# Kernel optimization log

Measured on AMD Instinct MI355X. Metric: run time of the kernel, lower is better.

## Reference

```python
import jax, jax.numpy as jnp
import numpy as np

B, T, D = 2, 2048, 2048
H = 8
DK = 256   # head_qk_dim
DV = 512   # head_v_dim
C = 64     # retention chunk size
EPS = 1e-5
ROPE_BASE = 10000.0


def _rotary(x):
    # x: [B, T, H, DK], non-interleaved (rotate-half) rotary over full head dim
    half = DK // 2
    inv_freq = 1.0 / (ROPE_BASE ** (jnp.arange(0, DK, 2, dtype=jnp.float32) / DK))
    freqs = jnp.arange(T, dtype=jnp.float32)[:, None] * inv_freq[None, :]  # [T, half]
    cos = jnp.cos(freqs)[None, :, None, :].astype(x.dtype)
    sin = jnp.sin(freqs)[None, :, None, :].astype(x.dtype)
    x1, x2 = x[..., :half], x[..., half:]
    return jnp.concatenate([x1 * cos - x2 * sin, x2 * cos + x1 * sin], axis=-1)


def setup_inputs() -> dict:
    key = jax.random.key(0)
    ks = jax.random.split(key, 6)
    s = 2.0 ** (-2.5) * (2.0 / 2048.0) ** 0.5  # xavier_uniform-ish scale, gain 2^-2.5
    return {
        "hidden_states": jax.random.normal(ks[0], (B, T, D), jnp.float32),
        "Wq": jax.random.normal(ks[1], (H * DK, D), jnp.float32) * s,
        "Wk": jax.random.normal(ks[2], (H * DK, D), jnp.float32) * s,
        "Wv": jax.random.normal(ks[3], (H * DV, D), jnp.float32) * s,
        "Wg": jax.random.normal(ks[4], (H * DV, D), jnp.float32) * s,
        "Wo": jax.random.normal(ks[5], (D, H * DV), jnp.float32) * s,
        "g_norm_weight": jnp.ones((DV,), jnp.float32),
    }


def reference(hidden_states, Wq, Wk, Wv, Wg, Wo, g_norm_weight):
    x = hidden_states  # [B, T, D]
    q = (x @ Wq.T).reshape(B, T, H, DK)
    k = (x @ Wk.T).reshape(B, T, H, DK)
    q = _rotary(q)
    k = _rotary(k)
    q = q.transpose(0, 2, 1, 3) * (DK ** -0.5)        # [B, H, T, DK]
    k = k.transpose(0, 2, 1, 3)                       # [B, H, T, DK]
    v = (x @ Wv.T).reshape(B, T, H, DV).transpose(0, 2, 1, 3)  # [B, H, T, DV]

    # RetNet multi-scale per-head decay
    logb = jnp.log(1.0 - 2.0 ** (-5.0 - jnp.arange(H, dtype=jnp.float32)))  # [H]
    i = jnp.arange(C, dtype=jnp.float32)
    # intra-chunk decay mask b^{i-j} for i>=j: [H, C, C]
    Dmask = jnp.where(i[:, None] >= i[None, :],
                      jnp.exp(logb[:, None, None] * (i[:, None] - i[None, :])), 0.0)
    q_dec = jnp.exp(logb[:, None] * (i + 1.0))        # [H, C]  decay applied to q vs carried state
    k_dec = jnp.exp(logb[:, None] * (C - 1.0 - i))    # [H, C]  decay applied to k for state update
    chunk_dec = jnp.exp(logb * C)                     # [H]

    N = T // C
    qc = q.reshape(B, H, N, C, DK).transpose(2, 0, 1, 3, 4)  # [N, B, H, C, DK]
    kc = k.reshape(B, H, N, C, DK).transpose(2, 0, 1, 3, 4)
    vc = v.reshape(B, H, N, C, DV).transpose(2, 0, 1, 3, 4)

    def body(S, inp):
        qi, ki, vi = inp  # [B,H,C,DK], [B,H,C,DK], [B,H,C,DV]
        inter = jnp.einsum('bhcd,bhdv->bhcv', qi * q_dec[None, :, :, None], S)
        scores = jnp.einsum('bhcd,bhmd->bhcm', qi, ki) * Dmask[None]
        o = inter + jnp.einsum('bhcm,bhmv->bhcv', scores, vi)
        S_new = S * chunk_dec[None, :, None, None] + \
                jnp.einsum('bhcd,bhcv->bhdv', ki * k_dec[None, :, :, None], vi)
        return S_new, o

    S0 = jnp.zeros((B, H, DK, DV), x.dtype)
    _, oc = jax.lax.scan(body, S0, (qc, kc, vc))  # oc: [N, B, H, C, DV]
    o = oc.transpose(1, 2, 0, 3, 4).reshape(B, H, T, DV).transpose(0, 2, 1, 3)  # [B, T, H, DV]

    g = (x @ Wg.T).reshape(B, T, H, DV)
    # fused RMSNorm + swish gate (per head_v_dim)
    o_n = o * jax.lax.rsqrt(jnp.mean(o * o, axis=-1, keepdims=True) + EPS) * g_norm_weight
    o = o_n * (g * jax.nn.sigmoid(g))
    return o.reshape(B, T, H * DV) @ Wo.T  # [B, T, D]
```

## Files before the change

### kernel.cpp

```cpp
#include <hip/hip_runtime.h>


typedef unsigned short u16;
typedef unsigned int u32;
typedef short bf16x8 __attribute__((ext_vector_type(8)));
typedef short s16x4 __attribute__((ext_vector_type(4)));
typedef float f32x4 __attribute__((ext_vector_type(4)));
typedef u32 u32x2 __attribute__((ext_vector_type(2)));
typedef u32 u32x4 __attribute__((ext_vector_type(4)));

typedef __attribute__((address_space(3))) u32 lds_u32;
typedef __attribute__((address_space(1))) const u32 gbl_u32;

__device__ __forceinline__ float bf2f(u16 u) {
    union { u32 i; float f; } x; x.i = ((u32)u) << 16; return x.f;
}
__device__ __forceinline__ u16 f2bf(float f) {
    union { float f; u32 i; } x; x.f = f;
    u32 u = x.i;
    u += 0x7fffu + ((u >> 16) & 1u);
    return (u16)(u >> 16);
}
__device__ __forceinline__ f32x4 mfma16(bf16x8 a, bf16x8 b, f32x4 c) {
    return __builtin_amdgcn_mfma_f32_16x16x32_bf16(a, b, c, 0, 0, 0);
}
__device__ __forceinline__ void gload16(const u16* g, u16* lds) {
    __builtin_amdgcn_global_load_lds((gbl_u32*)(unsigned long long)g,
                                     (lds_u32*)(u32)(unsigned long long)lds, 16, 0, 0);
}

__global__ __launch_bounds__(256)
void cvt_bf16(const float* __restrict__ src, u16* __restrict__ dst)
{
    size_t i = ((size_t)blockIdx.x * 256 + threadIdx.x) * 8;
    f32x4 a = *(const f32x4*)(src + i);
    f32x4 b = *(const f32x4*)(src + i + 4);
    bf16x8 r;
#pragma unroll
    for (int j = 0; j < 4; j++) { r[j] = (short)f2bf(a[j]); r[j + 4] = (short)f2bf(b[j]); }
    *(bf16x8*)(dst + i) = r;
}

template<bool CF32>
__global__ __launch_bounds__(256, 2)
void gemm_bt(const u16* __restrict__ A, const u16* __restrict__ Bm,
             void* __restrict__ Cv, int N, int K)
{
    __shared__ u16 Ab[128 * 64];
    __shared__ u16 Bb[128 * 64];
    const int tid = threadIdx.x;
    const int lane = tid & 63, wave = tid >> 6;
    const int quad = lane >> 4, l16 = lane & 15;
    const int tn = blockIdx.x, tm = blockIdx.y;
    const int wr = wave >> 1, wc = wave & 1;

    f32x4 acc[4][4];
#pragma unroll
    for (int i = 0; i < 4; i++)
#pragma unroll
        for (int j = 0; j < 4; j++) acc[i][j] = (f32x4){0.f, 0.f, 0.f, 0.f};

    const u16* Abase = A + (size_t)tm * 128 * K;
    const u16* Bbase = Bm + (size_t)tn * 128 * K;
    const int rsub = lane >> 3, csub = (lane & 7) * 8;

    for (int k0 = 0; k0 < K; k0 += 64) {
        __syncthreads();
#pragma unroll
        for (int i = 0; i < 4; i++) {
            int chunk = wave * 4 + i;
            int r = chunk * 8 + rsub;
            gload16(Abase + (size_t)r * K + k0 + csub, Ab + chunk * 512);
            gload16(Bbase + (size_t)r * K + k0 + csub, Bb + chunk * 512);
        }
        __syncthreads();
#pragma unroll
        for (int kc = 0; kc < 2; kc++) {
            bf16x8 af[4], bfr[4];
#pragma unroll
            for (int mt = 0; mt < 4; mt++)
                af[mt] = *(const bf16x8*)(Ab + (wr * 64 + mt * 16 + l16) * 64 + kc * 32 + quad * 8);
#pragma unroll
            for (int nt = 0; nt < 4; nt++)
                bfr[nt] = *(const bf16x8*)(Bb + (wc * 64 + nt * 16 + l16) * 64 + kc * 32 + quad * 8);
#pragma unroll
            for (int mt = 0; mt < 4; mt++)
#pragma unroll
                for (int nt = 0; nt < 4; nt++)
                    acc[mt][nt] = mfma16(af[mt], bfr[nt], acc[mt][nt]);
        }
    }
    const int row0 = tm * 128 + wr * 64 + quad * 4;
    const int col0 = tn * 128 + wc * 64 + l16;
#pragma unroll
    for (int mt = 0; mt < 4; mt++)
#pragma unroll
        for (int nt = 0; nt < 4; nt++)
#pragma unroll
            for (int r = 0; r < 4; r++) {
                size_t idx = (size_t)(row0 + mt * 16 + r) * N + col0 + nt * 16;
                if constexpr (CF32) ((float*)Cv)[idx] = acc[mt][nt][r];
                else                ((u16*)Cv)[idx]   = f2bf(acc[mt][nt][r]);
            }
}

__global__ __launch_bounds__(512, 2)
void gemm256(const u16* __restrict__ A, const u16* __restrict__ Bm,
             u16* __restrict__ C, int N, int K)
{
    __shared__ __align__(16) u16 As[2][2][256 * 32];
    __shared__ __align__(16) u16 Bs[2][2][256 * 32];
    const int tid = threadIdx.x;
    const int lane = tid & 63, wave = tid >> 6;
    const int quad = lane >> 4, l16 = lane & 15;
    const int wm = wave >> 2, wn = wave & 3;
    const int tn = blockIdx.x, tm = blockIdx.y;
    const int NTm1 = K / 64 - 1;
    const u16* Abase = A + (size_t)tm * 256 * K;
    const u16* Bbase = Bm + (size_t)tn * 256 * K;
    const int gr = tid >> 2;
    const int gc = (tid & 3) * 8;
    const int wv64 = wave * 64;

    f32x4 acc[8][4];
#pragma unroll
    for (int i = 0; i < 8; i++)
#pragma unroll
        for (int j = 0; j < 4; j++) acc[i][j] = (f32x4){0.f, 0.f, 0.f, 0.f};

    bf16x8 bq[8];
    bf16x8 af[4];

#define STAGE(arr, bf, kc, Gb, kt) do {                                         \
    int kt_ = (kt); kt_ = (kt_ > NTm1) ? NTm1 : kt_;                            \
    const u16* s_ = (Gb) + (size_t)gr * K + (size_t)kt_ * 64 + (kc) * 32 + gc;  \
    gload16(s_,                 &arr[bf][kc][wv64 * 8]);                        \
    gload16(s_ + (size_t)128 * K, &arr[bf][kc][(512 + wv64) * 8]);              \
} while (0)

#define LDA(bf, kc, mg) do {                                                    \
    _Pragma("unroll")                                                           \
    for (int j = 0; j < 4; j++)                                                 \
        af[j] = *(const bf16x8*)&As[bf][kc][(wm * 128 + (mg) * 64 + j * 16 + l16) * 32 + quad * 8]; \
} while (0)

#define LDB(bf) do {                                                            \
    _Pragma("unroll")                                                           \
    for (int kc_ = 0; kc_ < 2; kc_++)                                           \
        _Pragma("unroll")                                                       \
        for (int n_ = 0; n_ < 4; n_++)                                          \
            bq[kc_ * 4 + n_] = *(const bf16x8*)&Bs[bf][kc_][(wn * 64 + n_ * 16 + l16) * 32 + quad * 8]; \
} while (0)

#define MM16(kc, mg) do {                                                       \
    _Pragma("unroll")                                                           \
    for (int j = 0; j < 4; j++)                                                 \
        _Pragma("unroll")                                                       \
        for (int n_ = 0; n_ < 4; n_++)                                          \
            acc[(mg) * 4 + j][n_] = mfma16(af[j], bq[(kc) * 4 + n_], acc[(mg) * 4 + j][n_]); \
} while (0)

#define BAR   __builtin_amdgcn_s_barrier()
#define LGKM0 asm volatile("s_waitcnt lgkmcnt(0)" ::: "memory")
#define VM6   asm volatile("s_waitcnt vmcnt(6)" ::: "memory")
#define PRIO1 __builtin_amdgcn_s_setprio(1)
#define PRIO0 __builtin_amdgcn_s_setprio(0)

    STAGE(Bs, 0, 0, Bbase, 0);
    STAGE(Bs, 0, 1, Bbase, 0);
    STAGE(As, 0, 0, Abase, 0);
    STAGE(As, 0, 1, Abase, 0);
    asm volatile("s_waitcnt vmcnt(4)" ::: "memory");
    STAGE(Bs, 1, 0, Bbase, 1);
    STAGE(Bs, 1, 1, Bbase, 1);
    STAGE(As, 1, 0, Abase, 1);
    asm volatile("s_waitcnt vmcnt(6)" ::: "memory");
    BAR;

    const int NI = K / 128;
    for (int it = 0; it < NI; ++it) {
        const int t0 = 2 * it;
        LDB(0); LDA(0, 0, 0); STAGE(As, 1, 1, Abase, t0 + 1);
        BAR; LGKM0; PRIO1; MM16(0, 0); PRIO0; BAR;
        LDA(0, 0, 1); STAGE(Bs, 0, 0, Bbase, t0 + 2);
        BAR; LGKM0; PRIO1; MM16(0, 1); PRIO0; BAR;
        LDA(0, 1, 0); STAGE(Bs, 0, 1, Bbase, t0 + 2);
        BAR; LGKM0; PRIO1; MM16(1, 0); PRIO0; BAR;
        LDA(0, 1, 1); STAGE(As, 0, 0, Abase, t0 + 2);
        BAR; LGKM0; PRIO1; MM16(1, 1); PRIO0; VM6; BAR;
        LDB(1); LDA(1, 0, 0); STAGE(As, 0, 1, Abase, t0 + 2);
        BAR; LGKM0; PRIO1; MM16(0, 0); PRIO0; BAR;
        LDA(1, 0, 1); STAGE(Bs, 1, 0, Bbase, t0 + 3);
        BAR; LGKM0; PRIO1; MM16(0, 1); PRIO0; BAR;
        LDA(1, 1, 0); STAGE(Bs, 1, 1, Bbase, t0 + 3);
        BAR; LGKM0; PRIO1; MM16(1, 0); PRIO0; BAR;
        LDA(1, 1, 1); STAGE(As, 1, 0, Abase, t0 + 3);
        BAR; LGKM0; PRIO1; MM16(1, 1); PRIO0; VM6; BAR;
    }
    asm volatile("s_waitcnt vmcnt(0)" ::: "memory");

    const int row0 = tm * 256 + wm * 128 + quad * 4;
    const int col0 = tn * 256 + wn * 64 + l16;
#pragma unroll
    for (int mt = 0; mt < 8; mt++)
#pragma unroll
        for (int nt = 0; nt < 4; nt++)
#pragma unroll
            for (int r = 0; r < 4; r++)
                C[(size_t)(row0 + mt * 16 + r) * N + col0 + nt * 16] = f2bf(acc[mt][nt][r]);

#undef STAGE
#undef LDA
#undef LDB
#undef MM16
#undef BAR
#undef LGKM0
#undef VM6
#undef PRIO1
#undef PRIO0
}

__global__ __launch_bounds__(256, 2)
void rotary_scores(u16* __restrict__ q, const u16* __restrict__ k,
                   u16* __restrict__ kT, u16* __restrict__ P)
{
    __shared__ u16 qS[64 * 264];
    __shared__ u16 kS[64 * 264];
    const int tid = threadIdx.x;
    const int lane = tid & 63, wave = tid >> 6;
    const int quad = lane >> 4, l16 = lane & 15;
    const int bx = blockIdx.x;
    const int bh = bx & 15, n = bx >> 4;
    const int b = bh >> 3, h = bh & 7;
    const int t0 = n * 64;

    const int row = tid >> 2;
    const int j0 = (tid & 3) * 32;
    const size_t rowbase = (size_t)(b * 2048 + t0 + row) * 4096 + h * 256;
    const float tpos = (float)(t0 + row);
#pragma unroll
    for (int i = 0; i < 4; i++) {
        int j = j0 + i * 8;
        bf16x8 x1 = *(const bf16x8*)(q + rowbase + j);
        bf16x8 x2 = *(const bf16x8*)(q + rowbase + j + 128);
        bf16x8 y1 = *(const bf16x8*)(k + rowbase + j);
        bf16x8 y2 = *(const bf16x8*)(k + rowbase + j + 128);
        bf16x8 o1, o2, p1, p2;
#pragma unroll
        for (int e = 0; e < 8; e++) {
            float inv = expf((-9.210340371976184f / 128.f) * (float)(j + e));
            float ang = tpos * inv;
            float sv = sinf(ang), cv = cosf(ang);
            float a = bf2f((u16)x1[e]), bb = bf2f((u16)x2[e]);
            o1[e] = (short)f2bf((a * cv - bb * sv) * 0.0625f);
            o2[e] = (short)f2bf((bb * cv + a * sv) * 0.0625f);
            float e1 = bf2f((u16)y1[e]), e2 = bf2f((u16)y2[e]);
            p1[e] = (short)f2bf(e1 * cv - e2 * sv);
            p2[e] = (short)f2bf(e2 * cv + e1 * sv);
        }
        *(bf16x8*)(q + rowbase + j)       = o1;
        *(bf16x8*)(q + rowbase + j + 128) = o2;
        *(bf16x8*)(qS + row * 264 + j)       = o1;
        *(bf16x8*)(qS + row * 264 + j + 128) = o2;
        *(bf16x8*)(kS + row * 264 + j)       = p1;
        *(bf16x8*)(kS + row * 264 + j + 128) = p2;
    }
    __syncthreads();

    const float logb = logf(1.0f - exp2f(-5.0f - (float)h));
    f32x4 sc[4];
#pragma unroll
    for (int i = 0; i < 4; i++) sc[i] = (f32x4){0.f, 0.f, 0.f, 0.f};
#pragma unroll
    for (int kc = 0; kc < 8; kc++) {
        bf16x8 af = *(const bf16x8*)(qS + (wave * 16 + l16) * 264 + kc * 32 + quad * 8);
#pragma unroll
        for (int mt = 0; mt < 4; mt++) {
            bf16x8 bk = *(const bf16x8*)(kS + (mt * 16 + l16) * 264 + kc * 32 + quad * 8);
            sc[mt] = mfma16(af, bk, sc[mt]);
        }
    }
    u16* Pb = P + ((size_t)(bh * 32 + n)) * 64 * 64;
#pragma unroll
    for (int r = 0; r < 4; r++) {
        int cr = wave * 16 + quad * 4 + r;
        float rowe = __expf(logb * (float)(cr - 63));
#pragma unroll
        for (int mt = 0; mt < 4; mt++) {
            int m = mt * 16 + l16;
            float val = (cr >= m) ? sc[mt][r] * rowe : 0.0f;
            Pb[cr * 64 + m] = f2bf(val);
        }
    }

    const int d = tid;
    u16* dst = kT + ((size_t)(bh * 256 + d)) * 2048 + t0;
#pragma unroll
    for (int g8 = 0; g8 < 8; g8++) {
        bf16x8 w;
#pragma unroll
        for (int e = 0; e < 8; e++) w[e] = (short)kS[(g8 * 8 + e) * 264 + d];
        *(bf16x8*)(dst + g8 * 8) = w;
    }
}

__global__ __launch_bounds__(512, 2)
void retention(const u16* __restrict__ Q, const u16* __restrict__ KT,
               const u16* __restrict__ V, const u16* __restrict__ P,
               u16* __restrict__ O)
{
    __shared__ u16 St[2][32 * 264];
    __shared__ u16 vsT[2][32 * 72];

    const int tid = threadIdx.x;
    const int lane = tid & 63, wave = tid >> 6;
    const int quad = lane >> 4, l16 = lane & 15;
    const int bx = blockIdx.x;
    const int bh = bx & 15, vt = bx >> 4;
    const int b = bh >> 3, h = bh & 7;
    const int cgrp = wave >> 1, vhalf = wave & 1;

    const float logb = logf(1.0f - exp2f(-5.0f - (float)h));
    const float cdec = __expf(logb * 64.0f);

    int cr[4];
    float qdecr[4];
#pragma unroll
    for (int r = 0; r < 4; r++) {
        cr[r] = cgrp * 16 + quad * 4 + r;
        qdecr[r] = __expf(logb * (float)(cr[r] + 1));
    }
    const int mv = tid >> 3;
    const int vc4 = (tid & 7) * 4;
    const float kdv = __expf(logb * (float)(63 - mv));

    for (int i = tid; i < 32 * 264; i += 512) { St[0][i] = 0; St[1][i] = 0; }

    const u16* Qp  = Q  + (size_t)(b * 2048 + cgrp * 16 + l16) * 4096 + h * 256 + quad * 8;
    const u16* KTp = KT + (size_t)(bh * 256 + wave * 32 + l16) * 2048 + quad * 8;
    const u16* Pp  = P  + ((size_t)(bh * 32) * 64 + cgrp * 16 + l16) * 64 + quad * 8;
    const u16* Vp  = V  + (size_t)(b * 2048 + mv) * 4096 + h * 512 + vt * 32 + vc4;

    f32x4 Sacc[2][2];
#pragma unroll
    for (int dt = 0; dt < 2; dt++)
#pragma unroll
        for (int nt = 0; nt < 2; nt++) Sacc[dt][nt] = (f32x4){0.f, 0.f, 0.f, 0.f};

    bf16x8 qfA[8], qfB[8], ktA[4], ktB[4], pfA[2], pfB[2];
    u32x2 vvA, vvB;

#define LOADSET(nn, qf, kt, pf, vvn, nv) do {                                   \
    const int nL = (nn), vL = (nv);                                             \
    _Pragma("unroll")                                                           \
    for (int kc = 0; kc < 8; kc++)                                              \
        qf[kc] = *(const bf16x8*)(Qp + (size_t)nL * (64 * 4096) + kc * 32);     \
    _Pragma("unroll")                                                           \
    for (int dt = 0; dt < 2; dt++)                                              \
        _Pragma("unroll")                                                       \
        for (int kc2 = 0; kc2 < 2; kc2++)                                       \
            kt[dt * 2 + kc2] = *(const bf16x8*)(KTp + dt * (16 * 2048) + nL * 64 + kc2 * 32); \
    _Pragma("unroll")                                                           \
    for (int kc2 = 0; kc2 < 2; kc2++)                                           \
        pf[kc2] = *(const bf16x8*)(Pp + (size_t)nL * (64 * 64) + kc2 * 32);     \
    vvn = *(const u32x2*)(Vp + (size_t)vL * (64 * 4096));                       \
} while (0)

    u32x2 vv0 = *(const u32x2*)(Vp);
    LOADSET(0, qfA, ktA, pfA, vvA, 1);
    {
        u16 e0 = (u16)(vv0[0] & 0xffff), e1 = (u16)(vv0[0] >> 16);
        u16 e2 = (u16)(vv0[1] & 0xffff), e3 = (u16)(vv0[1] >> 16);
        vsT[0][(vc4 + 0) * 72 + mv] = f2bf(bf2f(e0) * kdv);
        vsT[0][(vc4 + 1) * 72 + mv] = f2bf(bf2f(e1) * kdv);
        vsT[0][(vc4 + 2) * 72 + mv] = f2bf(bf2f(e2) * kdv);
        vsT[0][(vc4 + 3) * 72 + mv] = f2bf(bf2f(e3) * kdv);
    }

#define CHUNK(nn, qfC, ktC, pfC, vvC, qfN, ktN, pfN, vvN) do {                  \
    const int nC = (nn);                                                        \
    const int nP = (nC + 1 < 32) ? nC + 1 : 31;                                 \
    const int nV = (nC + 2 < 32) ? nC + 2 : 31;                                 \
    LOADSET(nP, qfN, ktN, pfN, vvN, nV);         \
    asm volatile("s_waitcnt lgkmcnt(0)" ::: "memory");                          \
    __builtin_amdgcn_s_barrier();                                               \
    __builtin_amdgcn_sched_barrier(0);                                          \
    {                                 \
        u16* vd = &vsT[(nC + 1) & 1][0];                                        \
        u16 e0 = (u16)(vvC[0] & 0xffff), e1 = (u16)(vvC[0] >> 16);              \
        u16 e2 = (u16)(vvC[1] & 0xffff), e3 = (u16)(vvC[1] >> 16);              \
        vd[(vc4 + 0) * 72 + mv] = f2bf(bf2f(e0) * kdv);                         \
        vd[(vc4 + 1) * 72 + mv] = f2bf(bf2f(e1) * kdv);                         \
        vd[(vc4 + 2) * 72 + mv] = f2bf(bf2f(e2) * kdv);                         \
        vd[(vc4 + 3) * 72 + mv] = f2bf(bf2f(e3) * kdv);                         \
    }                                                                           \
                        \
    f32x4 oacc = (f32x4){0.f, 0.f, 0.f, 0.f};                                   \
    _Pragma("unroll")                                                           \
    for (int kc = 0; kc < 8; kc++) {                                            \
        bf16x8 bs = *(const bf16x8*)(&St[(nC + 1) & 1][0]                       \
                     + (vhalf * 16 + l16) * 264 + kc * 32 + quad * 8);          \
        oacc = mfma16(qfC[kc], bs, oacc);                                       \
    }                                                                           \
                        \
    _Pragma("unroll")                                                           \
    for (int dt = 0; dt < 2; dt++)                                              \
        _Pragma("unroll")                                                       \
        for (int nt = 0; nt < 2; nt++)                                          \
            _Pragma("unroll")                                                   \
            for (int e = 0; e < 4; e++) Sacc[dt][nt][e] *= cdec;                \
    _Pragma("unroll")                                                           \
    for (int kc2 = 0; kc2 < 2; kc2++) {                                         \
        bf16x8 bv0 = *(const bf16x8*)(&vsT[nC & 1][0] + l16 * 72 + kc2 * 32 + quad * 8);        \
        bf16x8 bv1 = *(const bf16x8*)(&vsT[nC & 1][0] + (16 + l16) * 72 + kc2 * 32 + quad * 8); \
        _Pragma("unroll")                                                       \
        for (int dt = 0; dt < 2; dt++) {                                        \
            Sacc[dt][0] = mfma16(ktC[dt * 2 + kc2], bv0, Sacc[dt][0]);          \
            Sacc[dt][1] = mfma16(ktC[dt * 2 + kc2], bv1, Sacc[dt][1]);          \
        }                                                                       \
    }                                                                           \
                                              \
    _Pragma("unroll")                                                           \
    for (int r = 0; r < 4; r++) oacc[r] *= qdecr[r];                            \
    _Pragma("unroll")                                                           \
    for (int kc2 = 0; kc2 < 2; kc2++) {                                         \
        bf16x8 bv = *(const bf16x8*)(&vsT[nC & 1][0]                            \
                     + (vhalf * 16 + l16) * 72 + kc2 * 32 + quad * 8);          \
        oacc = mfma16(pfC[kc2], bv, oacc);                                      \
    }                                                                           \
    _Pragma("unroll")                                                           \
    for (int r = 0; r < 4; r++)                                                 \
        O[(size_t)(b * 2048 + nC * 64 + cr[r]) * 4096 + h * 512 + vt * 32       \
          + vhalf * 16 + l16] = f2bf(oacc[r]);                                  \
                                       \
    _Pragma("unroll")                                                           \
    for (int dt = 0; dt < 2; dt++)                                              \
        _Pragma("unroll")                                                       \
        for (int nt = 0; nt < 2; nt++) {                                        \
            s16x4 w;                                                            \
            _Pragma("unroll")                                                   \
            for (int r = 0; r < 4; r++) w[r] = (short)f2bf(Sacc[dt][nt][r]);    \
            *(s16x4*)(&St[nC & 1][0] + (nt * 16 + l16) * 264 + wave * 32        \
                      + dt * 16 + quad * 4) = w;                                \
        }                                                                       \
} while (0)

    for (int m = 0; m < 16; m++) {
        CHUNK(2 * m,     qfA, ktA, pfA, vvA, qfB, ktB, pfB, vvB);
        CHUNK(2 * m + 1, qfB, ktB, pfB, vvB, qfA, ktA, pfA, vvA);
    }
#undef CHUNK
#undef LOADSET
}

__global__ __launch_bounds__(256)
void norm_gate(const u16* __restrict__ O, const u16* __restrict__ G,
               const float* __restrict__ gw, u16* __restrict__ ON)
{
    const int lane = threadIdx.x & 63;
    const size_t row = (size_t)blockIdx.x * 4 + (threadIdx.x >> 6);
    bf16x8 ov = *(const bf16x8*)(O + row * 512 + lane * 8);
    bf16x8 gv = *(const bf16x8*)(G + row * 512 + lane * 8);
    f32x4 w0 = *(const f32x4*)(gw + lane * 8);
    f32x4 w1 = *(const f32x4*)(gw + lane * 8 + 4);
    float of[8], gf[8];
    float ss = 0.f;
#pragma unroll
    for (int j = 0; j < 8; j++) {
        of[j] = bf2f((u16)ov[j]);
        gf[j] = bf2f((u16)gv[j]);
        ss += of[j] * of[j];
    }
#pragma unroll
    for (int off = 32; off > 0; off >>= 1) ss += __shfl_down(ss, off);
    ss = __shfl(ss, 0);
    const float rms = rsqrtf(ss * (1.0f / 512.0f) + 1e-5f);
    bf16x8 res;
#pragma unroll
    for (int j = 0; j < 8; j++) {
        float wj = (j < 4) ? w0[j] : w1[j - 4];
        float xn = of[j] * rms * wj;
        float sg = gf[j] / (1.f + __expf(-gf[j]));
        res[j] = (short)f2bf(xn * sg);
    }
    *(bf16x8*)(ON + row * 512 + lane * 8) = res;
}

extern "C" void kernel_launch(void* const* d_in, const int* in_sizes, int n_in,
                              void* d_out, int out_size, void* d_ws, size_t ws_size,
                              hipStream_t stream)
{
    const float* x  = (const float*)d_in[0];
    const float* Wq = (const float*)d_in[1];
    const float* Wk = (const float*)d_in[2];
    const float* Wv = (const float*)d_in[3];
    const float* Wg = (const float*)d_in[4];
    const float* Wo = (const float*)d_in[5];
    const float* gw = (const float*)d_in[6];
    float* out = (float*)d_out;

    const size_t M8 = (size_t)4096 * 2048;
    u16* Pb = (u16*)d_ws;
    u16* qk = Pb + (size_t)16 * 32 * 64 * 64;
    u16* kT = qk + 2 * M8;
    u16* v  = kT + M8;
    u16* o  = v + 2 * M8;
    u16* xb = o + 2 * M8;
    u16* g  = qk;
    u16* on = v;
    u16* wt = kT;

    dim3 blk(256, 1, 1), blk512(512, 1, 1);
    cvt_bf16<<<dim3(4096, 1, 1), blk, 0, stream>>>(x, xb);

    cvt_bf16<<<dim3(2048, 1, 1), blk, 0, stream>>>(Wq, wt);
    cvt_bf16<<<dim3(2048, 1, 1), blk, 0, stream>>>(Wk, wt + (size_t)2048 * 2048);
    gemm256<<<dim3(16, 16, 1), blk512, 0, stream>>>(xb, wt, qk, 4096, 2048);
    cvt_bf16<<<dim3(4096, 1, 1), blk, 0, stream>>>(Wv, wt);
    gemm256<<<dim3(16, 16, 1), blk512, 0, stream>>>(xb, wt, v, 4096, 2048);

    rotary_scores<<<dim3(512, 1, 1), blk, 0, stream>>>(qk, qk + 2048, kT, Pb);
    retention<<<dim3(256, 1, 1), blk512, 0, stream>>>(qk, kT, v, Pb, o);

    cvt_bf16<<<dim3(4096, 1, 1), blk, 0, stream>>>(Wg, kT);
    gemm256<<<dim3(16, 16, 1), blk512, 0, stream>>>(xb, kT, g, 4096, 2048);
    norm_gate<<<dim3(8192, 1, 1), blk, 0, stream>>>(o, g, gw, on);
    cvt_bf16<<<dim3(4096, 1, 1), blk, 0, stream>>>(Wo, kT);
    gemm_bt<true><<<dim3(16, 32, 1), blk, 0, stream>>>(on, kT, out, 2048, 4096);
}
```

Before: 601.8 us.

## Split retention into narrower value tiles and use pipelined GEMM for output projection

The retention kernel is restructured to 256 threads per block, each block covering 16 value columns instead of 32, which doubles the grid to 512 blocks. The state and value LDS buffers move to an MFMA-fragment-friendly flat layout with no padding. The output projection replaces the simple 128x128 gemm_bt with a new double-buffered 256x128 gemm256v that writes f32 output directly, reusing the staged-load schedule of gemm256. The aim is more parallelism in the sequential scan and better projection GEMM throughput. The cost is redundant Q/K/P loads per block in retention and higher register use.

```diff
diff --git a/kernel.cpp b/kernel.cpp
--- a/kernel.cpp
+++ b/kernel.cpp
@@ -7,7 +7,6 @@
 typedef short s16x4 __attribute__((ext_vector_type(4)));
 typedef float f32x4 __attribute__((ext_vector_type(4)));
 typedef u32 u32x2 __attribute__((ext_vector_type(2)));
-typedef u32 u32x4 __attribute__((ext_vector_type(4)));
 
 typedef __attribute__((address_space(3))) u32 lds_u32;
 typedef __attribute__((address_space(1))) const u32 gbl_u32;
@@ -39,69 +38,6 @@
 #pragma unroll
     for (int j = 0; j < 4; j++) { r[j] = (short)f2bf(a[j]); r[j + 4] = (short)f2bf(b[j]); }
     *(bf16x8*)(dst + i) = r;
-}
-
-template<bool CF32>
-__global__ __launch_bounds__(256, 2)
-void gemm_bt(const u16* __restrict__ A, const u16* __restrict__ Bm,
-             void* __restrict__ Cv, int N, int K)
-{
-    __shared__ u16 Ab[128 * 64];
-    __shared__ u16 Bb[128 * 64];
-    const int tid = threadIdx.x;
-    const int lane = tid & 63, wave = tid >> 6;
-    const int quad = lane >> 4, l16 = lane & 15;
-    const int tn = blockIdx.x, tm = blockIdx.y;
-    const int wr = wave >> 1, wc = wave & 1;
-
-    f32x4 acc[4][4];
-#pragma unroll
-    for (int i = 0; i < 4; i++)
-#pragma unroll
-        for (int j = 0; j < 4; j++) acc[i][j] = (f32x4){0.f, 0.f, 0.f, 0.f};
-
-    const u16* Abase = A + (size_t)tm * 128 * K;
-    const u16* Bbase = Bm + (size_t)tn * 128 * K;
-    const int rsub = lane >> 3, csub = (lane & 7) * 8;
-
-    for (int k0 = 0; k0 < K; k0 += 64) {
-        __syncthreads();
-#pragma unroll
-        for (int i = 0; i < 4; i++) {
-            int chunk = wave * 4 + i;
-            int r = chunk * 8 + rsub;
-            gload16(Abase + (size_t)r * K + k0 + csub, Ab + chunk * 512);
-            gload16(Bbase + (size_t)r * K + k0 + csub, Bb + chunk * 512);
-        }
-        __syncthreads();
-#pragma unroll
-        for (int kc = 0; kc < 2; kc++) {
-            bf16x8 af[4], bfr[4];
-#pragma unroll
-            for (int mt = 0; mt < 4; mt++)
-                af[mt] = *(const bf16x8*)(Ab + (wr * 64 + mt * 16 + l16) * 64 + kc * 32 + quad * 8);
-#pragma unroll
-            for (int nt = 0; nt < 4; nt++)
-                bfr[nt] = *(const bf16x8*)(Bb + (wc * 64 + nt * 16 + l16) * 64 + kc * 32 + quad * 8);
-#pragma unroll
-            for (int mt = 0; mt < 4; mt++)
-#pragma unroll
-                for (int nt = 0; nt < 4; nt++)
-                    acc[mt][nt] = mfma16(af[mt], bfr[nt], acc[mt][nt]);
-        }
-    }
-    const int row0 = tm * 128 + wr * 64 + quad * 4;
-    const int col0 = tn * 128 + wc * 64 + l16;
-#pragma unroll
-    for (int mt = 0; mt < 4; mt++)
-#pragma unroll
-        for (int nt = 0; nt < 4; nt++)
-#pragma unroll
-            for (int r = 0; r < 4; r++) {
-                size_t idx = (size_t)(row0 + mt * 16 + r) * N + col0 + nt * 16;
-                if constexpr (CF32) ((float*)Cv)[idx] = acc[mt][nt][r];
-                else                ((u16*)Cv)[idx]   = f2bf(acc[mt][nt][r]);
-            }
 }
 
 __global__ __launch_bounds__(512, 2)
@@ -213,6 +149,115 @@
 #undef LDA
 #undef LDB
 #undef MM16
+}
+
+__global__ __launch_bounds__(512, 2)
+void gemm256v(const u16* __restrict__ A, const u16* __restrict__ Bm,
+              float* __restrict__ C, int N, int K)
+{
+    __shared__ __align__(16) u16 As[2][2][256 * 32];
+    __shared__ __align__(16) u16 Bs[2][2][128 * 32];
+    const int tid = threadIdx.x;
+    const int lane = tid & 63, wave = tid >> 6;
+    const int quad = lane >> 4, l16 = lane & 15;
+    const int wm = wave >> 2, wn = wave & 3;
+    const int tn = blockIdx.x, tm = blockIdx.y;
+    const int NTm1 = K / 64 - 1;
+    const u16* Abase = A + (size_t)tm * 256 * K;
+    const u16* Bbase = Bm + (size_t)tn * 128 * K;
+    const int gr = tid >> 2;
+    const int gc = (tid & 3) * 8;
+    const int wv64 = wave * 64;
+
+    f32x4 acc[8][2];
+#pragma unroll
+    for (int i = 0; i < 8; i++)
+#pragma unroll
+        for (int j = 0; j < 2; j++) acc[i][j] = (f32x4){0.f, 0.f, 0.f, 0.f};
+
+    bf16x8 bq[4];
+    bf16x8 af[4];
+
+#define STAGEA(bf, kc, kt) do {                                                 \
+    int kt_ = (kt); kt_ = (kt_ > NTm1) ? NTm1 : kt_;                            \
+    const u16* s_ = Abase + (size_t)gr * K + (size_t)kt_ * 64 + (kc) * 32 + gc; \
+    gload16(s_,                   &As[bf][kc][wv64 * 8]);                       \
+    gload16(s_ + (size_t)128 * K, &As[bf][kc][(512 + wv64) * 8]);               \
+} while (0)
+
+#define STAGEB(bf, kc, kt) do {                                                 \
+    int kt_ = (kt); kt_ = (kt_ > NTm1) ? NTm1 : kt_;                            \
+    const u16* s_ = Bbase + (size_t)gr * K + (size_t)kt_ * 64 + (kc) * 32 + gc; \
+    gload16(s_, &Bs[bf][kc][wv64 * 8]);                                         \
+} while (0)
+
+#define LDAv(bf, kc, mg) do {                                                   \
+    _Pragma("unroll")                                                           \
+    for (int j = 0; j < 4; j++)                                                 \
+        af[j] = *(const bf16x8*)&As[bf][kc][(wm * 128 + (mg) * 64 + j * 16 + l16) * 32 + quad * 8]; \
+} while (0)
+
+#define LDBv(bf) do {                                                           \
+    _Pragma("unroll")                                                           \
+    for (int kc_ = 0; kc_ < 2; kc_++)                                           \
+        _Pragma("unroll")                                                       \
+        for (int n_ = 0; n_ < 2; n_++)                                          \
+            bq[kc_ * 2 + n_] = *(const bf16x8*)&Bs[bf][kc_][(wn * 32 + n_ * 16 + l16) * 32 + quad * 8]; \
+} while (0)
+
+#define MM8(kc, mg) do {                                                        \
+    _Pragma("unroll")                                                           \
+    for (int j = 0; j < 4; j++)                                                 \
+        _Pragma("unroll")                                                       \
+        for (int n_ = 0; n_ < 2; n_++)                                          \
+            acc[(mg) * 4 + j][n_] = mfma16(af[j], bq[(kc) * 2 + n_], acc[(mg) * 4 + j][n_]); \
+} while (0)
+
+#define VM4 asm volatile("s_waitcnt vmcnt(4)" ::: "memory")
+
+    STAGEB(0, 0, 0); STAGEB(0, 1, 0); STAGEA(0, 0, 0); STAGEA(0, 1, 0);
+    STAGEB(1, 0, 1); STAGEB(1, 1, 1); STAGEA(1, 0, 1);
+    VM4;
+    BAR;
+
+    const int NI = K / 128;
+    for (int it = 0; it < NI; ++it) {
+        const int t0 = 2 * it;
+        LDBv(0); LDAv(0, 0, 0); STAGEA(1, 1, t0 + 1);
+        BAR; LGKM0; PRIO1; MM8(0, 0); PRIO0; BAR;
+        LDAv(0, 0, 1); STAGEB(0, 0, t0 + 2);
+        BAR; LGKM0; PRIO1; MM8(0, 1); PRIO0; BAR;
+        LDAv(0, 1, 0); STAGEB(0, 1, t0 + 2);
+        BAR; LGKM0; PRIO1; MM8(1, 0); PRIO0; BAR;
+        LDAv(0, 1, 1); STAGEA(0, 0, t0 + 2);
+        BAR; LGKM0; PRIO1; MM8(1, 1); PRIO0; VM4; BAR;
+        LDBv(1); LDAv(1, 0, 0); STAGEA(0, 1, t0 + 2);
+        BAR; LGKM0; PRIO1; MM8(0, 0); PRIO0; BAR;
+        LDAv(1, 0, 1); STAGEB(1, 0, t0 + 3);
+        BAR; LGKM0; PRIO1; MM8(0, 1); PRIO0; BAR;
+        LDAv(1, 1, 0); STAGEB(1, 1, t0 + 3);
+        BAR; LGKM0; PRIO1; MM8(1, 0); PRIO0; BAR;
+        LDAv(1, 1, 1); STAGEA(1, 0, t0 + 3);
+        BAR; LGKM0; PRIO1; MM8(1, 1); PRIO0; VM4; BAR;
+    }
+    asm volatile("s_waitcnt vmcnt(0)" ::: "memory");
+
+    const int row0 = tm * 256 + wm * 128 + quad * 4;
+    const int col0 = tn * 128 + wn * 32 + l16;
+#pragma unroll
+    for (int mt = 0; mt < 8; mt++)
+#pragma unroll
+        for (int nt = 0; nt < 2; nt++)
+#pragma unroll
+            for (int r = 0; r < 4; r++)
+                C[(size_t)(row0 + mt * 16 + r) * N + col0 + nt * 16] = acc[mt][nt][r];
+
+#undef STAGEA
+#undef STAGEB
+#undef LDAv
+#undef LDBv
+#undef MM8
+#undef VM4
 #undef BAR
 #undef LGKM0
 #undef VM6
@@ -304,13 +349,13 @@
     }
 }
 
-__global__ __launch_bounds__(512, 2)
+__global__ __launch_bounds__(256, 2)
 void retention(const u16* __restrict__ Q, const u16* __restrict__ KT,
                const u16* __restrict__ V, const u16* __restrict__ P,
                u16* __restrict__ O)
 {
-    __shared__ u16 St[2][32 * 264];
-    __shared__ u16 vsT[2][32 * 72];
+    __shared__ __align__(16) u16 Stf[2][4096];
+    __shared__ __align__(16) u16 vsf[2][1024];
 
     const int tid = threadIdx.x;
     const int lane = tid & 63, wave = tid >> 6;
@@ -318,36 +363,30 @@
     const int bx = blockIdx.x;
     const int bh = bx & 15, vt = bx >> 4;
     const int b = bh >> 3, h = bh & 7;
-    const int cgrp = wave >> 1, vhalf = wave & 1;
 
     const float logb = logf(1.0f - exp2f(-5.0f - (float)h));
     const float cdec = __expf(logb * 64.0f);
-
-    int cr[4];
     float qdecr[4];
 #pragma unroll
-    for (int r = 0; r < 4; r++) {
-        cr[r] = cgrp * 16 + quad * 4 + r;
-        qdecr[r] = __expf(logb * (float)(cr[r] + 1));
-    }
-    const int mv = tid >> 3;
-    const int vc4 = (tid & 7) * 4;
-    const float kdv = __expf(logb * (float)(63 - mv));
-
-    for (int i = tid; i < 32 * 264; i += 512) { St[0][i] = 0; St[1][i] = 0; }
-
-    const u16* Qp  = Q  + (size_t)(b * 2048 + cgrp * 16 + l16) * 4096 + h * 256 + quad * 8;
-    const u16* KTp = KT + (size_t)(bh * 256 + wave * 32 + l16) * 2048 + quad * 8;
-    const u16* Pp  = P  + ((size_t)(bh * 32) * 64 + cgrp * 16 + l16) * 64 + quad * 8;
-    const u16* Vp  = V  + (size_t)(b * 2048 + mv) * 4096 + h * 512 + vt * 32 + vc4;
-
-    f32x4 Sacc[2][2];
-#pragma unroll
-    for (int dt = 0; dt < 2; dt++)
-#pragma unroll
-        for (int nt = 0; nt < 2; nt++) Sacc[dt][nt] = (f32x4){0.f, 0.f, 0.f, 0.f};
-
-    bf16x8 qfA[8], qfB[8], ktA[4], ktB[4], pfA[2], pfB[2];
+    for (int r = 0; r < 4; r++)
+        qdecr[r] = __expf(logb * (float)(wave * 16 + quad * 4 + r + 1));
+    const int w4 = wave * 4;
+    const float kdv = __expf(logb * (float)(63 - lane));
+    const int vwb = (((lane >> 5) * 4 + ((lane >> 3) & 3)) * 16 + w4) * 8 + (lane & 7);
+
+    for (int i = tid; i < 4096; i += 256) { Stf[0][i] = 0; Stf[1][i] = 0; }
+
+    const u16* Qp  = Q  + (size_t)(b * 2048 + wave * 16 + l16) * 4096 + h * 256 + quad * 8;
+    const u16* KTp = KT + (size_t)(bh * 256 + wave * 64 + l16) * 2048 + quad * 8;
+    const u16* Pp  = P  + ((size_t)(bh * 32) * 64 + wave * 16 + l16) * 64 + quad * 8;
+    const u16* Vp  = V  + (size_t)(b * 2048 + lane) * 4096 + h * 512 + vt * 16 + w4;
+    u16* Ob = O + (size_t)(b * 2048 + wave * 16 + quad * 4) * 4096 + h * 512 + vt * 16 + l16;
+
+    f32x4 Sacc[4];
+#pragma unroll
+    for (int dt = 0; dt < 4; dt++) Sacc[dt] = (f32x4){0.f, 0.f, 0.f, 0.f};
+
+    bf16x8 qfA[8], qfB[8], ktA[8], ktB[8], pfA[2], pfB[2];
     u32x2 vvA, vvB;
 
 #define LOADSET(nn, qf, kt, pf, vvn, nv) do {                                   \
@@ -356,93 +395,78 @@
     for (int kc = 0; kc < 8; kc++)                                              \
         qf[kc] = *(const bf16x8*)(Qp + (size_t)nL * (64 * 4096) + kc * 32);     \
     _Pragma("unroll")                                                           \
-    for (int dt = 0; dt < 2; dt++)                                              \
+    for (int dt = 0; dt < 4; dt++)                                              \
         _Pragma("unroll")                                                       \
         for (int kc2 = 0; kc2 < 2; kc2++)                                       \
-            kt[dt * 2 + kc2] = *(const bf16x8*)(KTp + dt * (16 * 2048) + nL * 64 + kc2 * 32); \
+            kt[dt * 2 + kc2] = *(const bf16x8*)(KTp + dt * (16 * 2048)          \
+                                  + (size_t)nL * 64 + kc2 * 32);                \
     _Pragma("unroll")                                                           \
     for (int kc2 = 0; kc2 < 2; kc2++)                                           \
         pf[kc2] = *(const bf16x8*)(Pp + (size_t)nL * (64 * 64) + kc2 * 32);     \
     vvn = *(const u32x2*)(Vp + (size_t)vL * (64 * 4096));                       \
 } while (0)
 
+#define STAGEVS(buf, vvC) do {                                                  \
+    u16* vd = &vsf[buf][0];                                                     \
+    u16 e0 = (u16)(vvC[0] & 0xffff), e1 = (u16)(vvC[0] >> 16);                  \
+    u16 e2 = (u16)(vvC[1] & 0xffff), e3 = (u16)(vvC[1] >> 16);                  \
+    vd[vwb + 0 * 8] = f2bf(bf2f(e0) * kdv);                                     \
+    vd[vwb + 1 * 8] = f2bf(bf2f(e1) * kdv);                                     \
+    vd[vwb + 2 * 8] = f2bf(bf2f(e2) * kdv);                                     \
+    vd[vwb + 3 * 8] = f2bf(bf2f(e3) * kdv);                                     \
+} while (0)
+
     u32x2 vv0 = *(const u32x2*)(Vp);
     LOADSET(0, qfA, ktA, pfA, vvA, 1);
-    {
-        u16 e0 = (u16)(vv0[0] & 0xffff), e1 = (u16)(vv0[0] >> 16);
-        u16 e2 = (u16)(vv0[1] & 0xffff), e3 = (u16)(vv0[1] >> 16);
-        vsT[0][(vc4 + 0) * 72 + mv] = f2bf(bf2f(e0) * kdv);
-        vsT[0][(vc4 + 1) * 72 + mv] = f2bf(bf2f(e1) * kdv);
-        vsT[0][(vc4 + 2) * 72 + mv] = f2bf(bf2f(e2) * kdv);
-        vsT[0][(vc4 + 3) * 72 + mv] = f2bf(bf2f(e3) * kdv);
-    }
+    STAGEVS(0, vv0);
 
 #define CHUNK(nn, qfC, ktC, pfC, vvC, qfN, ktN, pfN, vvN) do {                  \
     const int nC = (nn);                                                        \
     const int nP = (nC + 1 < 32) ? nC + 1 : 31;                                 \
     const int nV = (nC + 2 < 32) ? nC + 2 : 31;                                 \
-    LOADSET(nP, qfN, ktN, pfN, vvN, nV);         \
+    LOADSET(nP, qfN, ktN, pfN, vvN, nV);                   \
     asm volatile("s_waitcnt lgkmcnt(0)" ::: "memory");                          \
     __builtin_amdgcn_s_barrier();                                               \
     __builtin_amdgcn_sched_barrier(0);                                          \
-    {                                 \
-        u16* vd = &vsT[(nC + 1) & 1][0];                                        \
-        u16 e0 = (u16)(vvC[0] & 0xffff), e1 = (u16)(vvC[0] >> 16);              \
-        u16 e2 = (u16)(vvC[1] & 0xffff), e3 = (u16)(vvC[1] >> 16);              \
-        vd[(vc4 + 0) * 72 + mv] = f2bf(bf2f(e0) * kdv);                         \
-        vd[(vc4 + 1) * 72 + mv] = f2bf(bf2f(e1) * kdv);                         \
-        vd[(vc4 + 2) * 72 + mv] = f2bf(bf2f(e2) * kdv);                         \
-        vd[(vc4 + 3) * 72 + mv] = f2bf(bf2f(e3) * kdv);                         \
-    }                                                                           \
-                        \
+    STAGEVS((nC + 1) & 1, vvC);                                    \
+                       \
     f32x4 oacc = (f32x4){0.f, 0.f, 0.f, 0.f};                                   \
     _Pragma("unroll")                                                           \
     for (int kc = 0; kc < 8; kc++) {                                            \
-        bf16x8 bs = *(const bf16x8*)(&St[(nC + 1) & 1][0]                       \
-                     + (vhalf * 16 + l16) * 264 + kc * 32 + quad * 8);          \
+        bf16x8 bs = *(const bf16x8*)&Stf[(nC + 1) & 1][(kc * 4 + quad) * 128 + l16 * 8]; \
         oacc = mfma16(qfC[kc], bs, oacc);                                       \
     }                                                                           \
-                        \
-    _Pragma("unroll")                                                           \
-    for (int dt = 0; dt < 2; dt++)                                              \
-        _Pragma("unroll")                                                       \
-        for (int nt = 0; nt < 2; nt++)                                          \
-            _Pragma("unroll")                                                   \
-            for (int e = 0; e < 4; e++) Sacc[dt][nt][e] *= cdec;                \
-    _Pragma("unroll")                                                           \
-    for (int kc2 = 0; kc2 < 2; kc2++) {                                         \
-        bf16x8 bv0 = *(const bf16x8*)(&vsT[nC & 1][0] + l16 * 72 + kc2 * 32 + quad * 8);        \
-        bf16x8 bv1 = *(const bf16x8*)(&vsT[nC & 1][0] + (16 + l16) * 72 + kc2 * 32 + quad * 8); \
-        _Pragma("unroll")                                                       \
-        for (int dt = 0; dt < 2; dt++) {                                        \
-            Sacc[dt][0] = mfma16(ktC[dt * 2 + kc2], bv0, Sacc[dt][0]);          \
-            Sacc[dt][1] = mfma16(ktC[dt * 2 + kc2], bv1, Sacc[dt][1]);          \
-        }                                                                       \
+                                        \
+    bf16x8 bv0 = *(const bf16x8*)&vsf[nC & 1][(0 * 4 + quad) * 128 + l16 * 8];  \
+    bf16x8 bv1 = *(const bf16x8*)&vsf[nC & 1][(1 * 4 + quad) * 128 + l16 * 8];  \
+                                      \
+    _Pragma("unroll")                                                           \
+    for (int dt = 0; dt < 4; dt++)                                              \
+        _Pragma("unroll")                                                       \
+        for (int e = 0; e < 4; e++) Sacc[dt][e] *= cdec;                        \
+    _Pragma("unroll")                                                           \
+    for (int dt = 0; dt < 4; dt++) {                                            \
+        Sacc[dt] = mfma16(ktC[dt * 2 + 0], bv0, Sacc[dt]);                      \
+        Sacc[dt] = mfma16(ktC[dt * 2 + 1], bv1, Sacc[dt]);                      \
     }                                                                           \
                                               \
     _Pragma("unroll")                                                           \
     for (int r = 0; r < 4; r++) oacc[r] *= qdecr[r];                            \
-    _Pragma("unroll")                                                           \
-    for (int kc2 = 0; kc2 < 2; kc2++) {                                         \
-        bf16x8 bv = *(const bf16x8*)(&vsT[nC & 1][0]                            \
-                     + (vhalf * 16 + l16) * 72 + kc2 * 32 + quad * 8);          \
-        oacc = mfma16(pfC[kc2], bv, oacc);                                      \
+    oacc = mfma16(pfC[0], bv0, oacc);                                           \
+    oacc = mfma16(pfC[1], bv1, oacc);                                           \
+    _Pragma("unroll")                                                           \
+    for (int r = 0; r < 4; r++)                                                 \
+        Ob[(size_t)(nC * 64 + r) * 4096] = f2bf(oacc[r]);                       \
+                               \
+    _Pragma("unroll")                                                           \
+    for (int dt = 0; dt < 4; dt++) {                                            \
+        s16x4 w;                                                                \
+        _Pragma("unroll")                                                       \
+        for (int r = 0; r < 4; r++) w[r] = (short)f2bf(Sacc[dt][r]);            \
+        const int kct = 2 * wave + (dt >> 1);                                   \
+        const int qt  = (2 * dt + (quad >> 1)) & 3;                             \
+        *(s16x4*)&Stf[nC & 1][(kct * 4 + qt) * 128 + l16 * 8 + 4 * (quad & 1)] = w; \
     }                                                                           \
-    _Pragma("unroll")                                                           \
-    for (int r = 0; r < 4; r++)                                                 \
-        O[(size_t)(b * 2048 + nC * 64 + cr[r]) * 4096 + h * 512 + vt * 32       \
-          + vhalf * 16 + l16] = f2bf(oacc[r]);                                  \
-                                       \
-    _Pragma("unroll")                                                           \
-    for (int dt = 0; dt < 2; dt++)                                              \
-        _Pragma("unroll")                                                       \
-        for (int nt = 0; nt < 2; nt++) {                                        \
-            s16x4 w;                                                            \
-            _Pragma("unroll")                                                   \
-            for (int r = 0; r < 4; r++) w[r] = (short)f2bf(Sacc[dt][nt][r]);    \
-            *(s16x4*)(&St[nC & 1][0] + (nt * 16 + l16) * 264 + wave * 32        \
-                      + dt * 16 + quad * 4) = w;                                \
-        }                                                                       \
 } while (0)
 
     for (int m = 0; m < 16; m++) {
@@ -450,6 +474,7 @@
         CHUNK(2 * m + 1, qfB, ktB, pfB, vvB, qfA, ktA, pfA, vvA);
     }
 #undef CHUNK
+#undef STAGEVS
 #undef LOADSET
 }
 
@@ -520,11 +545,11 @@
     gemm256<<<dim3(16, 16, 1), blk512, 0, stream>>>(xb, wt, v, 4096, 2048);
 
     rotary_scores<<<dim3(512, 1, 1), blk, 0, stream>>>(qk, qk + 2048, kT, Pb);
-    retention<<<dim3(256, 1, 1), blk512, 0, stream>>>(qk, kT, v, Pb, o);
+    retention<<<dim3(512, 1, 1), blk, 0, stream>>>(qk, kT, v, Pb, o);
 
     cvt_bf16<<<dim3(4096, 1, 1), blk, 0, stream>>>(Wg, kT);
     gemm256<<<dim3(16, 16, 1), blk512, 0, stream>>>(xb, kT, g, 4096, 2048);
     norm_gate<<<dim3(8192, 1, 1), blk, 0, stream>>>(o, g, gw, on);
     cvt_bf16<<<dim3(4096, 1, 1), blk, 0, stream>>>(Wo, kT);
-    gemm_bt<true><<<dim3(16, 32, 1), blk, 0, stream>>>(on, kT, out, 2048, 4096);
-}
+    gemm256v<<<dim3(16, 16, 1), blk512, 0, stream>>>(on, kT, out, 2048, 4096);
+}
```

Result: slower. 621.5 us (+3.3%).
